# Optimization experiments

Hardware: AMD Instinct MI355X
Metric: run time of the kernel (lower is better)

The kernel has to match this reference:

```python
import math
import jax, jax.numpy as jnp
import numpy as np

NUM_HEADS = 16
D_MODEL = 1024
B, S = 1, 4096


def setup_inputs() -> dict:
    key = jax.random.key(0)
    ks = jax.random.split(key, 10)
    sc = 1.0 / math.sqrt(D_MODEL)
    # causal mask: 1.0 where masked (strictly upper triangular), 0.0 elsewhere
    causal = jnp.triu(jnp.ones((S, S), dtype=jnp.float32), k=1)
    return {
        "query": jax.random.normal(ks[0], (B, S, D_MODEL), dtype=jnp.float32),
        "mask": jnp.broadcast_to(causal, (B, S, S)),
        "Wq": jax.random.normal(ks[1], (D_MODEL, D_MODEL), dtype=jnp.float32) * sc,
        "bq": jax.random.normal(ks[2], (D_MODEL,), dtype=jnp.float32) * sc,
        "Wk": jax.random.normal(ks[3], (D_MODEL, D_MODEL), dtype=jnp.float32) * sc,
        "bk": jax.random.normal(ks[4], (D_MODEL,), dtype=jnp.float32) * sc,
        "Wv": jax.random.normal(ks[5], (D_MODEL, D_MODEL), dtype=jnp.float32) * sc,
        "bv": jax.random.normal(ks[6], (D_MODEL,), dtype=jnp.float32) * sc,
        "Wo": jax.random.normal(ks[7], (D_MODEL, D_MODEL), dtype=jnp.float32) * sc,
        "bo": jax.random.normal(ks[8], (D_MODEL,), dtype=jnp.float32) * sc,
    }


def _split_heads(x, H, dh):
    # [B,S,D] -> [B,H,S,dh]; head h owns channels [h*dh:(h+1)*dh] (matches the
    # module's transpose->reshape->transpose trick, which equals the contiguous split)
    b, s, _ = x.shape
    return x.reshape(b, s, H, dh).transpose(0, 2, 1, 3)


def reference(query, mask, Wq, bq, Wk, bk, Wv, bv, Wo, bo):
    H = NUM_HEADS
    B_, S_, D = query.shape
    dh = D // H
    q = _split_heads(query @ Wq.T + bq, H, dh)   # [B,H,S,dh]
    k = _split_heads(query @ Wk.T + bk, H, dh)   # self-attention: key = query
    v = _split_heads(query @ Wv.T + bv, H, dh)
    # materialized scores [B,H,S,S]
    scores = jnp.einsum("bhqd,bhkd->bhqk", q, k)
    # mask applied BEFORE the 1/sqrt(d_head) scaling, faithful to the source
    scores = scores + mask[:, None, :, :] * (-1e9)
    attn = jax.nn.softmax(scores / math.sqrt(dh), axis=-1)  # [B,H,S,S]
    out = jnp.einsum("bhqk,bhkd->bhqd", attn, v)            # [B,H,S,dh]
    combined = out.transpose(0, 2, 1, 3).reshape(B_, S_, D)  # [B,S,D]
    return combined @ Wo.T + bo
```

## Files before the change

kernel.cpp:

```cpp
#include <hip/hip_runtime.h>

typedef __bf16 bf16x8 __attribute__((ext_vector_type(8)));
typedef __bf16 bf16x4 __attribute__((ext_vector_type(4)));
typedef float f32x4 __attribute__((ext_vector_type(4)));
typedef unsigned u32x2 __attribute__((ext_vector_type(2)));
typedef unsigned u32x4 __attribute__((ext_vector_type(4)));

typedef const __attribute__((address_space(1))) void* as1_cvp;
typedef __attribute__((address_space(3))) void* as3_vp;
__device__ __forceinline__ void g2l16(const void* g, void* l) {
  __builtin_amdgcn_global_load_lds((as1_cvp)(uintptr_t)g, (as3_vp)(uintptr_t)l, 16, 0, 0);
}

__device__ __forceinline__ unsigned pk2(float lo, float hi) {
  unsigned short l = __builtin_bit_cast(unsigned short, (__bf16)lo);
  unsigned short h = __builtin_bit_cast(unsigned short, (__bf16)hi);
  return (unsigned)l | ((unsigned)h << 16);
}

__global__ __launch_bounds__(256) void cast_all(const float* __restrict__ q,
                                                const float* __restrict__ wq,
                                                const float* __restrict__ wk,
                                                const float* __restrict__ wv,
                                                const float* __restrict__ wo,
                                                __bf16* __restrict__ xb,
                                                __bf16* __restrict__ wqkv,
                                                __bf16* __restrict__ wob, float qs) {
  const int y = blockIdx.y;
  const float* src;
  __bf16* dst;
  int n4;
  float s = 1.0f;
  if (y == 0) {
    src = q; dst = xb; n4 = 1048576;
  } else if (y == 1) {
    src = wq; dst = wqkv; n4 = 262144; s = qs;
  } else if (y == 2) {
    src = wk; dst = wqkv + 1048576; n4 = 262144;
  } else if (y == 3) {
    src = wv; dst = wqkv + 2097152; n4 = 262144;
  } else {
    src = wo; dst = wob; n4 = 262144;
  }
  for (int idx = blockIdx.x * 256 + threadIdx.x; idx < n4; idx += gridDim.x * 256) {
    float4 f = reinterpret_cast<const float4*>(src)[idx];
    bf16x4 t;
    t.x = (__bf16)(f.x * s); t.y = (__bf16)(f.y * s);
    t.z = (__bf16)(f.z * s); t.w = (__bf16)(f.w * s);
    reinterpret_cast<bf16x4*>(dst)[idx] = t;
  }
}

__global__ __launch_bounds__(512, 2) void gemm8p(const __bf16* __restrict__ A,
                                                 const __bf16* __restrict__ B,
                                                 const float* __restrict__ b0,
                                                 const float* __restrict__ b1,
                                                 const float* __restrict__ b2,
                                                 __bf16* __restrict__ C,
                                                 __bf16* __restrict__ Vt,
                                                 int K, int ldc, float qs) {
  __shared__ __align__(16) __bf16 Alds[2][256][64];
  __shared__ __align__(16) __bf16 Blds[2][256][64];
  const int tid = threadIdx.x;
  const int wave = tid >> 6, lane = tid & 63;
  const int wm = wave >> 2, wn = wave & 3;
  const int mlane = lane & 15, quad = lane >> 4;
  const int m7 = mlane & 7;
  const int nwg = (int)(gridDim.x * gridDim.y);
  const int lin = (int)(blockIdx.y * gridDim.x + blockIdx.x);
  const int sl = (lin & 7) * (nwg >> 3) + (lin >> 3);
  const int bx = sl % (int)gridDim.x, by = sl / (int)gridDim.x;
  const int m0 = bx * 256, n0 = by * 256;

  f32x4 acc[8][4] = {};

  size_t aoff[2], boff[2];
  int ldso[2];
#pragma unroll
  for (int j = 0; j < 2; j++) {
    int c = j * 512 + tid, r = c >> 3, slo = c & 7;
    aoff[j] = ((size_t)(m0 + r) * K + (size_t)((slo ^ (r & 7)) * 8)) * 2;
    boff[j] = ((size_t)(n0 + r) * K + (size_t)((slo ^ (r & 7)) * 8)) * 2;
    ldso[j] = c * 16;
  }
  const char* Ag = (const char*)A;
  const char* Bg = (const char*)B;
  char* Ad = (char*)&Alds[0][0][0];
  char* Bd = (char*)&Blds[0][0][0];
  const size_t ghalf = (size_t)128 * K * 2;

  auto stA = [&](int t, int h) {
#pragma unroll
    for (int j = 0; j < 2; j++)
      g2l16(Ag + aoff[j] + (size_t)h * ghalf + (size_t)t * 128,
            Ad + ((t & 1) << 15) + (h << 14) + ldso[j]);
  };
  auto stB = [&](int t, int h) {
#pragma unroll
    for (int j = 0; j < 2; j++)
      g2l16(Bg + boff[j] + (size_t)h * ghalf + (size_t)t * 128,
            Bd + ((t & 1) << 15) + (h << 14) + ldso[j]);
  };

  auto bar = [] {
    asm volatile("" ::: "memory");
    __builtin_amdgcn_s_barrier();
    asm volatile("" ::: "memory");
  };

  bf16x8 af[4][2], bfrL[2][2], bfrH[2][2];
  auto ldA = [&](int buf, int mh) {
#pragma unroll
    for (int mt = 0; mt < 4; mt++)
#pragma unroll
      for (int s = 0; s < 2; s++)
        af[mt][s] = *reinterpret_cast<const bf16x8*>(
            &Alds[buf][mh * 128 + wm * 64 + mt * 16 + mlane][((4 * s + quad) ^ m7) * 8]);
  };
  auto ldB = [&](int buf, int nh, bf16x8 (&bf)[2][2]) {
#pragma unroll
    for (int nt = 0; nt < 2; nt++)
#pragma unroll
      for (int s = 0; s < 2; s++)
        bf[nt][s] = *reinterpret_cast<const bf16x8*>(
            &Blds[buf][nh * 128 + wn * 32 + nt * 16 + mlane][((4 * s + quad) ^ m7) * 8]);
  };
  auto mma = [&](int mh, int nh, bf16x8 (&bf)[2][2]) {
    __builtin_amdgcn_s_setprio(1);
#pragma unroll
    for (int mt = 0; mt < 4; mt++)
#pragma unroll
      for (int nt = 0; nt < 2; nt++)
#pragma unroll
        for (int s = 0; s < 2; s++)
          acc[mh * 4 + mt][nh * 2 + nt] = __builtin_amdgcn_mfma_f32_16x16x32_bf16(
              af[mt][s], bf[nt][s], acc[mh * 4 + mt][nh * 2 + nt], 0, 0, 0);
    __builtin_amdgcn_s_setprio(0);
  };

  const int nk = K >> 6;
  const int nit = nk >> 1;

  stA(0, 0); stB(0, 0); stA(0, 1); stB(0, 1); stA(1, 0); stB(1, 0);
  asm volatile("s_waitcnt vmcnt(8)" ::: "memory");
  bar();

  for (int i = 0; i < nit; ++i) {
    const int t1 = 2 * i + 1, t2 = 2 * i + 2, t3 = 2 * i + 3;
    const bool last = (i == nit - 1);
    ldA(0, 0); ldB(0, 0, bfrL);
    stA(t1, 1); stB(t1, 1);
    asm volatile("s_waitcnt vmcnt(8)" ::: "memory");
    bar(); mma(0, 0, bfrL); bar();
    ldB(0, 1, bfrH);
    bar(); mma(0, 1, bfrH); bar();
    ldA(0, 1);
    if (t2 < nk) stA(t2, 0);
    bar(); mma(1, 0, bfrL); bar();
    if (t2 < nk) stB(t2, 0);
    if (last) { asm volatile("s_waitcnt vmcnt(4)" ::: "memory"); }
    else      { asm volatile("s_waitcnt vmcnt(8)" ::: "memory"); }
    bar(); mma(1, 1, bfrH); bar();
    ldA(1, 0); ldB(1, 0, bfrL);
    if (t2 < nk) { stA(t2, 1); stB(t2, 1); }
    if (last) { asm volatile("s_waitcnt vmcnt(0)" ::: "memory"); }
    else      { asm volatile("s_waitcnt vmcnt(8)" ::: "memory"); }
    bar(); mma(0, 0, bfrL); bar();
    ldB(1, 1, bfrH);
    bar(); mma(0, 1, bfrH); bar();
    ldA(1, 1);
    if (t3 < nk) stA(t3, 0);
    bar(); mma(1, 0, bfrL); bar();
    if (t3 < nk) stB(t3, 0);
    if (!last) { asm volatile("s_waitcnt vmcnt(8)" ::: "memory"); }
    bar(); mma(1, 1, bfrH); bar();
  }

  const int region = n0 >> 10;
  const float* bp = region == 0 ? b0 : (region == 1 ? b1 : b2);
  const float bs = (region == 0) ? qs : 1.0f;
  float bvs[4];
#pragma unroll
  for (int ni = 0; ni < 4; ni++) {
    int nh = ni >> 1, nt = ni & 1;
    bvs[ni] = bp[(n0 + nh * 128 + wn * 32 + nt * 16 + mlane) & 1023] * bs;
  }

  if (region == 2) {
#pragma unroll
    for (int mi = 0; mi < 8; mi++) {
      int mh = mi >> 2, mt = mi & 3;
      int row0 = m0 + mh * 128 + wm * 64 + mt * 16 + quad * 4;
#pragma unroll
      for (int ni = 0; ni < 4; ni++) {
        int nh = ni >> 1, nt = ni & 1;
        int vcol = (n0 + nh * 128 + wn * 32 + nt * 16 + mlane) & 1023;
        bf16x4 t;
#pragma unroll
        for (int r = 0; r < 4; r++) t[r] = (__bf16)(acc[mi][ni][r] + bvs[ni]);
        *reinterpret_cast<bf16x4*>(&Vt[(size_t)vcol * 4096 + row0]) = t;
      }
    }
  } else {
#pragma unroll
    for (int mi = 0; mi < 8; mi++) {
      int mh = mi >> 2, mt = mi & 3;
#pragma unroll
      for (int ni = 0; ni < 4; ni++) {
        int nh = ni >> 1, nt = ni & 1;
        int col = n0 + nh * 128 + wn * 32 + nt * 16 + mlane;
#pragma unroll
        for (int r = 0; r < 4; r++) {
          int row = m0 + mh * 128 + wm * 64 + mt * 16 + quad * 4 + r;
          C[(size_t)row * ldc + col] = (__bf16)(acc[mi][ni][r] + bvs[ni]);
        }
      }
    }
  }
}

template <int BM, typename OUT_T>
__global__ __launch_bounds__(512, 4) void gemm_bt(const __bf16* __restrict__ A,
                                                  const __bf16* __restrict__ B,
                                                  const float* __restrict__ b0,
                                                  OUT_T* __restrict__ C,
                                                  int K, int ldc) {
  constexpr int MT = BM / 32;
  constexpr int AN = BM / 64;
  __shared__ __align__(16) __bf16 Alds[2][BM][64];
  __shared__ __align__(16) __bf16 Blds[2][128][64];
  const int tid = threadIdx.x;
  const int wave = tid >> 6, lane = tid & 63;
  const int wm = wave >> 2, wn = wave & 3;
  const int mlane = lane & 15, quad = lane >> 4;
  const int m7 = mlane & 7;
  const int nwg = (int)(gridDim.x * gridDim.y);
  const int lin = (int)(blockIdx.y * gridDim.x + blockIdx.x);
  const int sl = (lin & 7) * (nwg >> 3) + (lin >> 3);
  const int bx = sl % (int)gridDim.x, by = sl / (int)gridDim.x;
  const int m0 = bx * BM, n0 = by * 128;

  f32x4 acc[MT][2] = {};

  auto STAGE = [&](int k0, int buf) {
#pragma unroll
    for (int j = 0; j < AN; j++) {
      int c = j * 512 + tid;
      int r = c >> 3, slo = c & 7;
      g2l16(&A[(size_t)(m0 + r) * K + k0 + ((slo ^ (r & 7)) * 8)],
            &Alds[buf][0][0] + c * 8);
    }
#pragma unroll
    for (int j = 0; j < 2; j++) {
      int c = j * 512 + tid;
      int r = c >> 3, slo = c & 7;
      g2l16(&B[(size_t)(n0 + r) * K + k0 + ((slo ^ (r & 7)) * 8)],
            &Blds[buf][0][0] + c * 8);
    }
  };

  STAGE(0, 0);
  __syncthreads();
  const int nk = K >> 6;
  for (int t = 0; t < nk; ++t) {
    const int buf = t & 1;
    if (t + 1 < nk) STAGE((t + 1) << 6, buf ^ 1);
    bf16x8 af[MT][2], bfr[2][2];
#pragma unroll
    for (int mt = 0; mt < MT; mt++)
#pragma unroll
      for (int s = 0; s < 2; s++)
        af[mt][s] = *reinterpret_cast<const bf16x8*>(
            &Alds[buf][wm * (BM / 2) + mt * 16 + mlane][((4 * s + quad) ^ m7) * 8]);
#pragma unroll
    for (int nt = 0; nt < 2; nt++)
#pragma unroll
      for (int s = 0; s < 2; s++)
        bfr[nt][s] = *reinterpret_cast<const bf16x8*>(
            &Blds[buf][wn * 32 + nt * 16 + mlane][((4 * s + quad) ^ m7) * 8]);
#pragma unroll
    for (int mt = 0; mt < MT; mt++)
#pragma unroll
      for (int nt = 0; nt < 2; nt++)
#pragma unroll
        for (int s = 0; s < 2; s++)
          acc[mt][nt] = __builtin_amdgcn_mfma_f32_16x16x32_bf16(af[mt][s], bfr[nt][s],
                                                                acc[mt][nt], 0, 0, 0);
    __syncthreads();
  }

  float bvs[2];
#pragma unroll
  for (int nt = 0; nt < 2; nt++)
    bvs[nt] = b0[(n0 + wn * 32 + nt * 16 + mlane) & 1023];

#pragma unroll
  for (int mt = 0; mt < MT; mt++)
#pragma unroll
    for (int nt = 0; nt < 2; nt++) {
      int col = n0 + wn * 32 + nt * 16 + mlane;
#pragma unroll
      for (int r = 0; r < 4; r++) {
        int row = m0 + wm * (BM / 2) + mt * 16 + quad * 4 + r;
        C[(size_t)row * ldc + col] = (OUT_T)(acc[mt][nt][r] + bvs[nt]);
      }
    }
}

__global__ __launch_bounds__(512, 4) void flash_attn(const __bf16* __restrict__ QK,
                                                     const __bf16* __restrict__ Vt,
                                                     __bf16* __restrict__ O, int S) {
  const int LDQ = 2048, D = 1024;
  __shared__ __align__(16) char smem[65536];
  const int tid = threadIdx.x;
  const int wave = tid >> 6, lane = tid & 63;
  const int mlane = lane & 15, quad = lane >> 4;
  const int half = wave >> 2, rw = wave & 3;
  const int lin = (int)(blockIdx.y * 32 + blockIdx.x);
  const int sl = (lin & 7) * 64 + (lin >> 3);
  const int b = sl & 31, h = sl >> 5;
  const int m7 = mlane & 7;

  const __bf16* kgb[2];
  const __bf16* vgb[2];
  int kds[2], vds[2];
#pragma unroll
  for (int j = 0; j < 2; j++) {
    int c = j * 512 + tid;
    int r = c >> 3, sl2 = c & 7;
    kgb[j] = QK + (size_t)r * LDQ + 1024 + h * 64 + ((sl2 ^ (r & 7)) * 8);
    kds[j] = c * 16;
  }
#pragma unroll
  for (int j = 0; j < 2; j++) {
    int c = j * 512 + tid;
    int r = c >> 4, sl2 = c & 15;
    vgb[j] = Vt + (size_t)(h * 64 + r) * S + ((sl2 ^ (r & 15)) * 8);
    vds[j] = c * 16;
  }

  for (int pass = 0; pass < 2; ++pass) {
    const int qb = pass ? b : (63 - b);
    const int qbase = qb * 64 + rw * 16;
    const int qg = qbase + mlane;

    bf16x8 qf[2];
#pragma unroll
    for (int s = 0; s < 2; s++)
      qf[s] = *reinterpret_cast<const bf16x8*>(
          &QK[(size_t)(qbase + mlane) * LDQ + h * 64 + s * 32 + quad * 8]);

    f32x4 o[4] = {};
    float lsum = 0.f;

    const int nkb = qb / 2 + 1;

    auto STAGE = [&](int t, int buf) {
      char* kd = smem + buf * 16384;
      char* vd = smem + 32768 + buf * 16384;
      const size_t ko = (size_t)t * 128 * LDQ;
      const int vo = t * 128;
#pragma unroll
      for (int j = 0; j < 2; j++) g2l16(kgb[j] + ko, kd + kds[j]);
#pragma unroll
      for (int j = 0; j < 2; j++) g2l16(vgb[j] + vo, vd + vds[j]);
    };

    STAGE(0, 0);
    __syncthreads();

    for (int kb = 0; kb < nkb; ++kb) {
      const int buf = kb & 1;
      __bf16(*Klds)[64] = (__bf16(*)[64])(smem + buf * 16384);
      __bf16(*Vlds)[128] = (__bf16(*)[128])(smem + 32768 + buf * 16384);

      if (kb + 1 < nkb) STAGE(kb + 1, buf ^ 1);

      f32x4 sc[4];
      __builtin_amdgcn_s_setprio(1);
#pragma unroll
      for (int nt = 0; nt < 4; nt++) {
        f32x4 a = {};
#pragma unroll
        for (int s = 0; s < 2; s++) {
          bf16x8 bk = *reinterpret_cast<const bf16x8*>(
              &Klds[half * 64 + nt * 16 + mlane][((4 * s + quad) ^ m7) * 8]);
          a = __builtin_amdgcn_mfma_f32_16x16x32_bf16(bk, qf[s], a, 0, 0, 0);
        }
        sc[nt] = a;
      }
      __builtin_amdgcn_s_setprio(0);

      const bool maskTile = (kb == nkb - 1);
#pragma unroll
      for (int nt = 0; nt < 4; nt++) {
        if (maskTile) {
          const int kg0 = kb * 128 + half * 64 + nt * 16 + quad * 4;
#pragma unroll
          for (int r = 0; r < 4; r++)
            if (kg0 + r > qg) sc[nt][r] = -INFINITY;
        }
#pragma unroll
        for (int r = 0; r < 4; r++) {
          float p = __builtin_amdgcn_exp2f(sc[nt][r]);
          sc[nt][r] = p;
          lsum += p;
        }
      }

      unsigned w00 = pk2(sc[0][0], sc[0][1]), w01 = pk2(sc[0][2], sc[0][3]);
      unsigned w10 = pk2(sc[1][0], sc[1][1]), w11 = pk2(sc[1][2], sc[1][3]);
      unsigned w20 = pk2(sc[2][0], sc[2][1]), w21 = pk2(sc[2][2], sc[2][3]);
      unsigned w30 = pk2(sc[3][0], sc[3][1]), w31 = pk2(sc[3][2], sc[3][3]);

      u32x2 t0 = __builtin_amdgcn_permlane32_swap(w00, w10, false, false);
      u32x2 z02 = __builtin_amdgcn_permlane16_swap(t0.x, t0.y, false, false);
      u32x2 t1 = __builtin_amdgcn_permlane32_swap(w01, w11, false, false);
      u32x2 z13 = __builtin_amdgcn_permlane16_swap(t1.x, t1.y, false, false);
      u32x2 t2 = __builtin_amdgcn_permlane32_swap(w20, w30, false, false);
      u32x2 z02b = __builtin_amdgcn_permlane16_swap(t2.x, t2.y, false, false);
      u32x2 t3 = __builtin_amdgcn_permlane32_swap(w21, w31, false, false);
      u32x2 z13b = __builtin_amdgcn_permlane16_swap(t3.x, t3.y, false, false);
      u32x4 pf0u = {z02.x, z13.x, z02.y, z13.y};
      u32x4 pf1u = {z02b.x, z13b.x, z02b.y, z13b.y};
      bf16x8 pf[2] = {__builtin_bit_cast(bf16x8, pf0u), __builtin_bit_cast(bf16x8, pf1u)};

      __builtin_amdgcn_s_setprio(1);
#pragma unroll
      for (int s = 0; s < 2; s++) {
#pragma unroll
        for (int nt = 0; nt < 4; nt++) {
          bf16x8 vf = *reinterpret_cast<const bf16x8*>(
              &Vlds[nt * 16 + mlane][((half * 8 + s * 4 + quad) ^ mlane) * 8]);
          o[nt] = __builtin_amdgcn_mfma_f32_16x16x32_bf16(pf[s], vf, o[nt], 0, 0, 0);
        }
      }
      __builtin_amdgcn_s_setprio(0);
      __syncthreads();
    }

    lsum += __shfl_xor(lsum, 16, 64);
    lsum += __shfl_xor(lsum, 32, 64);

    float* osc = (float*)smem;
    float* lsc = (float*)(smem + 17408);
    if (lane < 16) lsc[half * 64 + rw * 16 + lane] = lsum;
    if (half == 1) {
      const int ob = (rw * 64 + lane) * 17;
#pragma unroll
      for (int nt = 0; nt < 4; nt++)
#pragma unroll
        for (int r = 0; r < 4; r++) osc[ob + nt * 4 + r] = o[nt][r];
    }
    __syncthreads();
    if (half == 0) {
      const int ob = (rw * 64 + lane) * 17;
#pragma unroll
      for (int nt = 0; nt < 4; nt++)
#pragma unroll
        for (int r = 0; r < 4; r++) o[nt][r] += osc[ob + nt * 4 + r];
#pragma unroll
      for (int r = 0; r < 4; r++) {
        float l = lsc[rw * 16 + quad * 4 + r] + lsc[64 + rw * 16 + quad * 4 + r];
        float inv = 1.0f / l;
        int row = qbase + quad * 4 + r;
#pragma unroll
        for (int nt = 0; nt < 4; nt++)
          O[(size_t)row * D + h * 64 + nt * 16 + mlane] = (__bf16)(o[nt][r] * inv);
      }
    }
    __syncthreads();
  }
}

extern "C" void kernel_launch(void* const* d_in, const int* in_sizes, int n_in,
                              void* d_out, int out_size, void* d_ws, size_t ws_size,
                              hipStream_t stream) {
  const float* query = (const float*)d_in[0];
  const float* Wq = (const float*)d_in[2];
  const float* bq = (const float*)d_in[3];
  const float* Wk = (const float*)d_in[4];
  const float* bk = (const float*)d_in[5];
  const float* Wv = (const float*)d_in[6];
  const float* bv = (const float*)d_in[7];
  const float* Wo = (const float*)d_in[8];
  const float* bo = (const float*)d_in[9];
  float* out = (float*)d_out;

  const int S = 4096, D = 1024;
  const float SCL = 0.125f * 1.44269504088896340736f;
  char* ws = (char*)d_ws;
  __bf16* Xb   = (__bf16*)(ws);
  __bf16* Cb   = (__bf16*)(ws);
  __bf16* Wqkv = (__bf16*)(ws + (8u << 20));
  __bf16* Wob  = (__bf16*)(ws + (14u << 20));
  __bf16* QKb  = (__bf16*)(ws + (16u << 20));
  __bf16* Vt   = (__bf16*)(ws + (32u << 20));

  cast_all<<<dim3(512, 5), 256, 0, stream>>>(query, Wq, Wk, Wv, Wo, Xb, Wqkv, Wob, SCL);

  gemm8p<<<dim3(S / 256, 3 * D / 256), 512, 0, stream>>>(
      Xb, Wqkv, bq, bk, bv, QKb, Vt, D, 2048, SCL);

  flash_attn<<<dim3(32, 16), 512, 0, stream>>>(QKb, Vt, Cb, S);

  gemm_bt<64, float><<<dim3(S / 64, D / 128), 512, 0, stream>>>(
      Cb, Wob, bo, out, D, D);
}
```

Measured before the change: 227.0 us.

## Load V fragments directly from global and skip fully masked causal half-tiles

V is no longer staged through LDS. Each wave reads its V^T MFMA operands directly from global memory into registers, and LDS shrinks to 32 KB, which could allow more resident blocks. Waves whose half of the 128-key tile lies entirely above the causal diagonal now skip QK, softmax and PV work. The cost is uncached-by-LDS global reads that are issued each iteration with less latency hiding, and wave divergence within a block.

```diff
diff --git a/kernel.cpp b/kernel.cpp
--- a/kernel.cpp
+++ b/kernel.cpp
@@ -311,7 +311,7 @@
                                                      const __bf16* __restrict__ Vt,
                                                      __bf16* __restrict__ O, int S) {
   const int LDQ = 2048, D = 1024;
-  __shared__ __align__(16) char smem[65536];
+  __shared__ __align__(16) char smem[32768];
   const int tid = threadIdx.x;
   const int wave = tid >> 6, lane = tid & 63;
   const int mlane = lane & 15, quad = lane >> 4;
@@ -322,8 +322,7 @@
   const int m7 = mlane & 7;
 
   const __bf16* kgb[2];
-  const __bf16* vgb[2];
-  int kds[2], vds[2];
+  int kds[2];
 #pragma unroll
   for (int j = 0; j < 2; j++) {
     int c = j * 512 + tid;
@@ -331,13 +330,7 @@
     kgb[j] = QK + (size_t)r * LDQ + 1024 + h * 64 + ((sl2 ^ (r & 7)) * 8);
     kds[j] = c * 16;
   }
-#pragma unroll
-  for (int j = 0; j < 2; j++) {
-    int c = j * 512 + tid;
-    int r = c >> 4, sl2 = c & 15;
-    vgb[j] = Vt + (size_t)(h * 64 + r) * S + ((sl2 ^ (r & 15)) * 8);
-    vds[j] = c * 16;
-  }
+  const __bf16* vb = Vt + (size_t)(h * 64 + mlane) * S + half * 64 + quad * 8;
 
   for (int pass = 0; pass < 2; ++pass) {
     const int qb = pass ? b : (63 - b);
@@ -355,87 +348,91 @@
 
     const int nkb = qb / 2 + 1;
 
-    auto STAGE = [&](int t, int buf) {
+    auto STAGEK = [&](int t, int buf) {
       char* kd = smem + buf * 16384;
-      char* vd = smem + 32768 + buf * 16384;
       const size_t ko = (size_t)t * 128 * LDQ;
-      const int vo = t * 128;
 #pragma unroll
       for (int j = 0; j < 2; j++) g2l16(kgb[j] + ko, kd + kds[j]);
-#pragma unroll
-      for (int j = 0; j < 2; j++) g2l16(vgb[j] + vo, vd + vds[j]);
     };
 
-    STAGE(0, 0);
+    STAGEK(0, 0);
     __syncthreads();
 
     for (int kb = 0; kb < nkb; ++kb) {
       const int buf = kb & 1;
       __bf16(*Klds)[64] = (__bf16(*)[64])(smem + buf * 16384);
-      __bf16(*Vlds)[128] = (__bf16(*)[128])(smem + 32768 + buf * 16384);
-
-      if (kb + 1 < nkb) STAGE(kb + 1, buf ^ 1);
-
-      f32x4 sc[4];
-      __builtin_amdgcn_s_setprio(1);
-#pragma unroll
-      for (int nt = 0; nt < 4; nt++) {
-        f32x4 a = {};
-#pragma unroll
-        for (int s = 0; s < 2; s++) {
-          bf16x8 bk = *reinterpret_cast<const bf16x8*>(
-              &Klds[half * 64 + nt * 16 + mlane][((4 * s + quad) ^ m7) * 8]);
-          a = __builtin_amdgcn_mfma_f32_16x16x32_bf16(bk, qf[s], a, 0, 0, 0);
+
+      if (kb + 1 < nkb) STAGEK(kb + 1, buf ^ 1);
+
+      const bool dead = (kb * 128 + half * 64) > (qbase + 15);
+      if (!dead) {
+        f32x4 sc[4];
+        __builtin_amdgcn_s_setprio(1);
+#pragma unroll
+        for (int nt = 0; nt < 4; nt++) {
+          f32x4 a = {};
+#pragma unroll
+          for (int s = 0; s < 2; s++) {
+            bf16x8 bk = *reinterpret_cast<const bf16x8*>(
+                &Klds[half * 64 + nt * 16 + mlane][((4 * s + quad) ^ m7) * 8]);
+            a = __builtin_amdgcn_mfma_f32_16x16x32_bf16(bk, qf[s], a, 0, 0, 0);
+          }
+          sc[nt] = a;
         }
-        sc[nt] = a;
+        __builtin_amdgcn_s_setprio(0);
+
+        bf16x8 vfr[2][4];
+#pragma unroll
+        for (int s = 0; s < 2; s++)
+#pragma unroll
+          for (int nt = 0; nt < 4; nt++)
+            vfr[s][nt] = *reinterpret_cast<const bf16x8*>(
+                vb + (size_t)nt * 16 * S + kb * 128 + s * 32);
+
+        const bool maskTile = (kb == nkb - 1);
+#pragma unroll
+        for (int nt = 0; nt < 4; nt++) {
+          if (maskTile) {
+            const int kg0 = kb * 128 + half * 64 + nt * 16 + quad * 4;
+#pragma unroll
+            for (int r = 0; r < 4; r++)
+              if (kg0 + r > qg) sc[nt][r] = -INFINITY;
+          }
+#pragma unroll
+          for (int r = 0; r < 4; r++) {
+            float p = __builtin_amdgcn_exp2f(sc[nt][r]);
+            sc[nt][r] = p;
+            lsum += p;
+          }
+        }
+
+        unsigned w00 = pk2(sc[0][0], sc[0][1]), w01 = pk2(sc[0][2], sc[0][3]);
+        unsigned w10 = pk2(sc[1][0], sc[1][1]), w11 = pk2(sc[1][2], sc[1][3]);
+        unsigned w20 = pk2(sc[2][0], sc[2][1]), w21 = pk2(sc[2][2], sc[2][3]);
+        unsigned w30 = pk2(sc[3][0], sc[3][1]), w31 = pk2(sc[3][2], sc[3][3]);
+
+        u32x2 t0 = __builtin_amdgcn_permlane32_swap(w00, w10, false, false);
+        u32x2 z02 = __builtin_amdgcn_permlane16_swap(t0.x, t0.y, false, false);
+        u32x2 t1 = __builtin_amdgcn_permlane32_swap(w01, w11, false, false);
+        u32x2 z13 = __builtin_amdgcn_permlane16_swap(t1.x, t1.y, false, false);
+        u32x2 t2 = __builtin_amdgcn_permlane32_swap(w20, w30, false, false);
+        u32x2 z02b = __builtin_amdgcn_permlane16_swap(t2.x, t2.y, false, false);
+        u32x2 t3 = __builtin_amdgcn_permlane32_swap(w21, w31, false, false);
+        u32x2 z13b = __builtin_amdgcn_permlane16_swap(t3.x, t3.y, false, false);
+        u32x4 pf0u = {z02.x, z13.x, z02.y, z13.y};
+        u32x4 pf1u = {z02b.x, z13b.x, z02b.y, z13b.y};
+        bf16x8 pf[2] = {__builtin_bit_cast(bf16x8, pf0u),
+                        __builtin_bit_cast(bf16x8, pf1u)};
+
+        __builtin_amdgcn_s_setprio(1);
+#pragma unroll
+        for (int s = 0; s < 2; s++)
+#pragma unroll
+          for (int nt = 0; nt < 4; nt++)
+            o[nt] = __builtin_amdgcn_mfma_f32_16x16x32_bf16(pf[s], vfr[s][nt], o[nt],
+                                                            0, 0, 0);
+        __builtin_amdgcn_s_setprio(0);
       }
-      __builtin_amdgcn_s_setprio(0);
-
-      const bool maskTile = (kb == nkb - 1);
-#pragma unroll
-      for (int nt = 0; nt < 4; nt++) {
-        if (maskTile) {
-          const int kg0 = kb * 128 + half * 64 + nt * 16 + quad * 4;
-#pragma unroll
-          for (int r = 0; r < 4; r++)
-            if (kg0 + r > qg) sc[nt][r] = -INFINITY;
-        }
-#pragma unroll
-        for (int r = 0; r < 4; r++) {
-          float p = __builtin_amdgcn_exp2f(sc[nt][r]);
-          sc[nt][r] = p;
-          lsum += p;
-        }
-      }
-
-      unsigned w00 = pk2(sc[0][0], sc[0][1]), w01 = pk2(sc[0][2], sc[0][3]);
-      unsigned w10 = pk2(sc[1][0], sc[1][1]), w11 = pk2(sc[1][2], sc[1][3]);
-      unsigned w20 = pk2(sc[2][0], sc[2][1]), w21 = pk2(sc[2][2], sc[2][3]);
-      unsigned w30 = pk2(sc[3][0], sc[3][1]), w31 = pk2(sc[3][2], sc[3][3]);
-
-      u32x2 t0 = __builtin_amdgcn_permlane32_swap(w00, w10, false, false);
-      u32x2 z02 = __builtin_amdgcn_permlane16_swap(t0.x, t0.y, false, false);
-      u32x2 t1 = __builtin_amdgcn_permlane32_swap(w01, w11, false, false);
-      u32x2 z13 = __builtin_amdgcn_permlane16_swap(t1.x, t1.y, false, false);
-      u32x2 t2 = __builtin_amdgcn_permlane32_swap(w20, w30, false, false);
-      u32x2 z02b = __builtin_amdgcn_permlane16_swap(t2.x, t2.y, false, false);
-      u32x2 t3 = __builtin_amdgcn_permlane32_swap(w21, w31, false, false);
-      u32x2 z13b = __builtin_amdgcn_permlane16_swap(t3.x, t3.y, false, false);
-      u32x4 pf0u = {z02.x, z13.x, z02.y, z13.y};
-      u32x4 pf1u = {z02b.x, z13b.x, z02b.y, z13b.y};
-      bf16x8 pf[2] = {__builtin_bit_cast(bf16x8, pf0u), __builtin_bit_cast(bf16x8, pf1u)};
-
-      __builtin_amdgcn_s_setprio(1);
-#pragma unroll
-      for (int s = 0; s < 2; s++) {
-#pragma unroll
-        for (int nt = 0; nt < 4; nt++) {
-          bf16x8 vf = *reinterpret_cast<const bf16x8*>(
-              &Vlds[nt * 16 + mlane][((half * 8 + s * 4 + quad) ^ mlane) * 8]);
-          o[nt] = __builtin_amdgcn_mfma_f32_16x16x32_bf16(pf[s], vf, o[nt], 0, 0, 0);
-        }
-      }
-      __builtin_amdgcn_s_setprio(0);
       __syncthreads();
     }
 
```

Measured after the change: 308.6 us. 35.9% more time.
